# Performance work log

Measured on AMD Instinct MI355X. Metric: run time of the kernel, lower is better.

The kernel has to match this reference:

```python
import jax, jax.numpy as jnp
import numpy as np

B, S, D = 8, 2048, 256
MASK_FILL = -1e9


def setup_inputs() -> dict:
    key = jax.random.key(0)
    kq, kk, kv = jax.random.split(key, 3)
    query = jax.random.normal(kq, (B, S, D), dtype=jnp.float32)
    k_ = jax.random.normal(kk, (B, S, D), dtype=jnp.float32)
    value = jax.random.normal(kv, (B, S, D), dtype=jnp.float32)
    # causal mask: True = masked (gets -1e9), broadcast over batch
    causal = jnp.triu(jnp.ones((S, S), dtype=bool), k=1)
    mask = jnp.broadcast_to(causal, (B, S, S))
    return {"query": query, "key": k_, "value": value, "mask": mask}


def reference(query, key, value, mask):
    d = jnp.asarray(query.shape[-1], dtype=query.dtype)
    # (B,S,S) = bmm(Q, K^T) / sqrt(D)
    attention = jnp.einsum('bqd,bkd->bqk', query, key) / jnp.sqrt(d)
    attention = jnp.where(mask, jnp.asarray(MASK_FILL, attention.dtype), attention)
    attention = jax.nn.softmax(attention, axis=2)
    # dropout p=0.0 -> identity
    out = jnp.einsum('bqk,bkd->bqd', attention, value)
    return out, attention
```

## Files before the change

kernel.cpp:

```cpp
#include <hip/hip_runtime.h>
#include <hip/hip_bf16.h>

typedef __attribute__((ext_vector_type(4))) float  f32x4;
typedef __attribute__((ext_vector_type(8))) __bf16 bf16x8;

constexpr int Bn = 8, Sn = 2048, Dn = 256;
#define SCALE 0.0625f

__device__ float  g_lpart[(size_t)Bn * Sn * 16];
__device__ __bf16 g_vt[(size_t)Bn * Dn * Sn];
__device__ __bf16 g_praw[(size_t)Bn * Sn * Sn];

__device__ __forceinline__ f32x4 mfma_bf16(bf16x8 a, bf16x8 b, f32x4 c) {
  return __builtin_amdgcn_mfma_f32_16x16x32_bf16(a, b, c, 0, 0, 0);
}

__device__ __forceinline__ bf16x8 cvt8(const float* p) {
  const f32x4* q = (const f32x4*)p;
  f32x4 u0 = q[0], u1 = q[1];
  bf16x8 r;
#pragma unroll
  for (int j = 0; j < 4; ++j) { r[j] = (__bf16)u0[j]; r[4 + j] = (__bf16)u1[j]; }
  return r;
}

__global__ __launch_bounds__(512) void k_qkvt(const float* __restrict__ Q,
                                              const float* __restrict__ K,
                                              const float* __restrict__ V) {
  __shared__ __align__(16) char lds[34816];
  int tid = threadIdx.x;
  int bx = blockIdx.x;

  if (bx < 1024) {
    __bf16 (*t)[65] = reinterpret_cast<__bf16(*)[65]>(lds);
    int b = bx >> 7, rem = bx & 127;
    int s0 = (rem >> 2) << 6, d0 = (rem & 3) << 6;
#pragma unroll
    for (int i = 0; i < 8; ++i) {
      int idx = tid + (i << 9);
      int r = idx >> 6, c = idx & 63;
      t[r][c] = (__bf16)V[((size_t)(b * Sn + s0 + r) << 8) + d0 + c];
    }
    __syncthreads();
#pragma unroll
    for (int i = 0; i < 8; ++i) {
      int idx = tid + (i << 9);
      int r = idx >> 6, c = idx & 63;
      g_vt[((size_t)(b * Dn + d0 + r) << 11) + s0 + c] = t[c][r];
    }
    return;
  }

  __bf16 (*Ab)[64] = reinterpret_cast<__bf16(*)[64]>(lds);
  __bf16 (*Bb)[64] = reinterpret_cast<__bf16(*)[64]>(lds + 16384);
  __bf16 (*pbuf)[136] = reinterpret_cast<__bf16(*)[136]>(lds);

  int w = tid >> 6, lane = tid & 63, g = lane >> 4, c = lane & 15;
  int mi = w >> 2, ni = w & 3;
  int bq = bx - 1024;
  int b = bq & 7;
  int idx = bq >> 3;
  int mt = 15 - (idx >> 4), nt = idx & 15;
  if (nt > mt) return;

  int grow0 = mt << 7, gcol0 = nt << 7;
  const float* Qb = Q + (size_t)(b * Sn) * Dn;
  const float* Kb = K + (size_t)(b * Sn) * Dn;

  int sr = tid >> 2, u0 = (tid & 3) << 1;
  const float* qs = Qb + (size_t)(grow0 + sr) * Dn + (u0 << 3);
  const float* ks = Kb + (size_t)(gcol0 + sr) * Dn + (u0 << 3);
  int su0 = (u0 ^ (sr & 7)) << 3, su1 = ((u0 + 1) ^ (sr & 7)) << 3;

  f32x4 acc[4][2];
#pragma unroll
  for (int m2 = 0; m2 < 4; ++m2)
#pragma unroll
    for (int n2 = 0; n2 < 2; ++n2) acc[m2][n2] = {0.f, 0.f, 0.f, 0.f};

  bf16x8 qa0 = cvt8(qs), qa1 = cvt8(qs + 8);
  bf16x8 ka0 = cvt8(ks), ka1 = cvt8(ks + 8);

  for (int kb = 0; kb < 4; ++kb) {
    *reinterpret_cast<bf16x8*>(&Ab[sr][su0]) = qa0;
    *reinterpret_cast<bf16x8*>(&Ab[sr][su1]) = qa1;
    *reinterpret_cast<bf16x8*>(&Bb[sr][su0]) = ka0;
    *reinterpret_cast<bf16x8*>(&Bb[sr][su1]) = ka1;
    __syncthreads();

    if (kb + 1 < 4) {
      int k0 = (kb + 1) << 6;
      qa0 = cvt8(qs + k0);
      qa1 = cvt8(qs + k0 + 8);
      ka0 = cvt8(ks + k0);
      ka1 = cvt8(ks + k0 + 8);
    }

#pragma unroll
    for (int dk = 0; dk < 2; ++dk) {
      bf16x8 af[4], bfr[2];
#pragma unroll
      for (int m2 = 0; m2 < 4; ++m2) {
        int rr = (mi << 6) + (m2 << 4) + c;
        int uu = (g + (dk << 2)) ^ (rr & 7);
        af[m2] = *reinterpret_cast<const bf16x8*>(&Ab[rr][uu << 3]);
      }
#pragma unroll
      for (int n2 = 0; n2 < 2; ++n2) {
        int rr = (ni << 5) + (n2 << 4) + c;
        int uu = (g + (dk << 2)) ^ (rr & 7);
        bfr[n2] = *reinterpret_cast<const bf16x8*>(&Bb[rr][uu << 3]);
      }
#pragma unroll
      for (int m2 = 0; m2 < 4; ++m2)
#pragma unroll
        for (int n2 = 0; n2 < 2; ++n2)
          acc[m2][n2] = mfma_bf16(af[m2], bfr[n2], acc[m2][n2]);
    }
    __syncthreads();
  }

  bool diag = (nt == mt);
#pragma unroll
  for (int m2 = 0; m2 < 4; ++m2) {
#pragma unroll
    for (int r = 0; r < 4; ++r) {
      int row_l = (mi << 6) + (m2 << 4) + (g << 2) + r;
#pragma unroll
      for (int n2 = 0; n2 < 2; ++n2) {
        int col_l = (ni << 5) + (n2 << 4) + c;
        float e = (!diag || col_l <= row_l) ? __expf(acc[m2][n2][r] * SCALE) : 0.f;
        pbuf[row_l][col_l] = (__bf16)e;
      }
    }
  }
  __syncthreads();

  {
    int r = tid >> 2, q = tid & 3;
    __bf16* dst =
        g_praw + ((size_t)b << 22) + ((size_t)(grow0 + r) << 11) + gcol0 + (q << 5);
    float s = 0.f;
#pragma unroll
    for (int i = 0; i < 4; ++i) {
      bf16x8 vv = *reinterpret_cast<const bf16x8*>(&pbuf[r][(q << 5) + (i << 3)]);
      *reinterpret_cast<bf16x8*>(dst + (i << 3)) = vv;
#pragma unroll
      for (int e = 0; e < 8; ++e) s += (float)vv[e];
    }
    s += __shfl_xor(s, 1, 64);
    s += __shfl_xor(s, 2, 64);
    if (q == 0) g_lpart[((size_t)b * Sn + grow0 + r) * 16 + nt] = s;
  }
}

__global__ __launch_bounds__(512, 4) void k_pv(float* __restrict__ P,
                                               float* __restrict__ O) {
  __shared__ __align__(16) __bf16 abuf[2][64][64];
  __shared__ __align__(16) __bf16 vbuf[2][128][64];
  __shared__ float linv_s[64];
  int tid = threadIdx.x;
  int w = tid >> 6, lane = tid & 63, g = lane >> 4, c = lane & 15;
  int mi = w >> 2, ni = w & 3;
  int b = blockIdx.x & 7;
  int idx = blockIdx.x >> 3;
  int dh = idx & 1;
  int mt = 31 - (idx >> 1);
  int row0 = mt << 6;
  int nc = mt + 1;
  const __bf16* prb = g_praw + ((size_t)b << 22);
  const __bf16* vtb = g_vt + ((size_t)(b * Dn + (dh << 7)) << 11);
  float* Pb = P + ((size_t)b << 22);

  if (tid < 64) {
    const f32x4* p = reinterpret_cast<const f32x4*>(
        g_lpart + ((size_t)(b << 11) + row0 + tid) * 16);
    f32x4 s = (p[0] + p[1]) + (p[2] + p[3]);
    linv_s[tid] = 1.f / ((s[0] + s[1]) + (s[2] + s[3]));
  }

  int sr = tid >> 3, su = tid & 7;
  const __bf16* sp = prb + ((size_t)(row0 + sr) << 11) + (su << 3);
  float* spw = Pb + ((size_t)(row0 + sr) << 11) + (su << 3);
  int swu = (su ^ (sr & 7)) << 3;
  int vr = tid >> 2, vu = (tid & 3) << 1;
  const __bf16* vpp = vtb + ((size_t)vr << 11) + (vu << 3);
  int swv0 = (vu ^ (vr & 7)) << 3, swv1 = ((vu + 1) ^ (vr & 7)) << 3;

  f32x4 acc[2][2];
#pragma unroll
  for (int m2 = 0; m2 < 2; ++m2)
#pragma unroll
    for (int n2 = 0; n2 < 2; ++n2) acc[m2][n2] = {0.f, 0.f, 0.f, 0.f};

  bf16x8 pr = *reinterpret_cast<const bf16x8*>(sp);
  bf16x8 vt0 = *reinterpret_cast<const bf16x8*>(vpp);
  bf16x8 vt1 = *reinterpret_cast<const bf16x8*>(vpp + 8);

  __syncthreads();
  float slv = linv_s[sr];

  for (int j = 0; j < nc; ++j) {
    int jb = j & 1;
    *reinterpret_cast<bf16x8*>(&abuf[jb][sr][swu]) = pr;
    *reinterpret_cast<bf16x8*>(&vbuf[jb][vr][swv0]) = vt0;
    *reinterpret_cast<bf16x8*>(&vbuf[jb][vr][swv1]) = vt1;
    if ((j >> 4) == dh) {
      f32x4 p0, p1;
#pragma unroll
      for (int e = 0; e < 4; ++e) {
        p0[e] = (float)pr[e] * slv;
        p1[e] = (float)pr[4 + e] * slv;
      }
      float* pw = spw + ((size_t)j << 6);
      *reinterpret_cast<f32x4*>(pw) = p0;
      *reinterpret_cast<f32x4*>(pw + 4) = p1;
    }
    __syncthreads();

    if (j + 1 < nc) {
      const __bf16* sp2 = sp + ((size_t)(j + 1) << 6);
      const __bf16* vp2 = vpp + ((size_t)(j + 1) << 6);
      pr = *reinterpret_cast<const bf16x8*>(sp2);
      vt0 = *reinterpret_cast<const bf16x8*>(vp2);
      vt1 = *reinterpret_cast<const bf16x8*>(vp2 + 8);
    }

#pragma unroll
    for (int kk = 0; kk < 2; ++kk) {
      int ua = (kk << 2) + g;
      int ar0 = (mi << 5) + c, ar1 = ar0 + 16;
      bf16x8 a0 = *reinterpret_cast<const bf16x8*>(
          &abuf[jb][ar0][(ua ^ (ar0 & 7)) << 3]);
      bf16x8 a1 = *reinterpret_cast<const bf16x8*>(
          &abuf[jb][ar1][(ua ^ (ar1 & 7)) << 3]);
      int dr0 = (ni << 5) + c, dr1 = dr0 + 16;
      bf16x8 b0 = *reinterpret_cast<const bf16x8*>(
          &vbuf[jb][dr0][(ua ^ (dr0 & 7)) << 3]);
      bf16x8 b1 = *reinterpret_cast<const bf16x8*>(
          &vbuf[jb][dr1][(ua ^ (dr1 & 7)) << 3]);
      acc[0][0] = mfma_bf16(a0, b0, acc[0][0]);
      acc[0][1] = mfma_bf16(a0, b1, acc[0][1]);
      acc[1][0] = mfma_bf16(a1, b0, acc[1][0]);
      acc[1][1] = mfma_bf16(a1, b1, acc[1][1]);
    }
  }

  {
    int zs = nc << 6, hlo = dh << 10;
    if (zs < hlo) zs = hlo;
    int zend = hlo + 1024;
    float* prow = Pb + ((size_t)(row0 + sr) << 11);
    f32x4 z = {0.f, 0.f, 0.f, 0.f};
    for (int col = zs + (su << 2); col < zend; col += 32)
      *reinterpret_cast<f32x4*>(prow + col) = z;
  }

#pragma unroll
  for (int m2 = 0; m2 < 2; ++m2)
#pragma unroll
    for (int n2 = 0; n2 < 2; ++n2)
#pragma unroll
      for (int r = 0; r < 4; ++r) {
        int rl = (mi << 5) + (m2 << 4) + (g << 2) + r;
        O[((size_t)(b * Sn + row0 + rl) << 8) + (dh << 7) + (ni << 5) +
          (n2 << 4) + c] = acc[m2][n2][r] * linv_s[rl];
      }
}

extern "C" void kernel_launch(void* const* d_in, const int* in_sizes, int n_in,
                              void* d_out, int out_size, void* d_ws, size_t ws_size,
                              hipStream_t stream) {
  const float* Q = (const float*)d_in[0];
  const float* K = (const float*)d_in[1];
  const float* V = (const float*)d_in[2];

  float* out  = (float*)d_out;
  float* attn = out + (size_t)Bn * Sn * Dn;

  hipLaunchKernelGGL(k_qkvt, dim3(3072), dim3(512), 0, stream, Q, K, V);
  hipLaunchKernelGGL(k_pv, dim3(512), dim3(512), 0, stream, attn, out);
}
```

Before: 86.64 us.

## Widen QK^T tiles to 128x256 with 1024-thread blocks and split loaders

The QK^T/exp kernel now computes 128x256 score tiles with 16 waves per block instead of 128x128 tiles with 8 waves. Half of the threads stage Q and the other half stage the wider K tile, so each Q tile is loaded and converted once per 256 columns instead of once per 128. The causal mask is now applied per element using global coordinates for any tile that crosses the diagonal, and the row-sum reduction is widened to 8 lanes. This reduces redundant Q traffic and block count, at the cost of more wasted work on tiles that straddle the diagonal, larger LDS use, and lower occupancy from 1024-thread blocks. It also changes how partial row sums are indexed, which the unseen PV kernel must match.

```diff
diff --git a/kernel.cpp b/kernel.cpp
--- a/kernel.cpp
+++ b/kernel.cpp
@@ -24,10 +24,10 @@
   return r;
 }
 
-__global__ __launch_bounds__(512) void k_qkvt(const float* __restrict__ Q,
-                                              const float* __restrict__ K,
-                                              const float* __restrict__ V) {
-  __shared__ __align__(16) char lds[34816];
+__global__ __launch_bounds__(1024) void k_qkvt(const float* __restrict__ Q,
+                                               const float* __restrict__ K,
+                                               const float* __restrict__ V) {
+  __shared__ __align__(16) char lds[67584];
   int tid = threadIdx.x;
   int bx = blockIdx.x;
 
@@ -36,91 +36,128 @@
     int b = bx >> 7, rem = bx & 127;
     int s0 = (rem >> 2) << 6, d0 = (rem & 3) << 6;
 #pragma unroll
-    for (int i = 0; i < 8; ++i) {
-      int idx = tid + (i << 9);
+    for (int i = 0; i < 4; ++i) {
+      int idx = tid + (i << 10);
       int r = idx >> 6, c = idx & 63;
       t[r][c] = (__bf16)V[((size_t)(b * Sn + s0 + r) << 8) + d0 + c];
     }
     __syncthreads();
 #pragma unroll
-    for (int i = 0; i < 8; ++i) {
-      int idx = tid + (i << 9);
+    for (int i = 0; i < 4; ++i) {
+      int idx = tid + (i << 10);
       int r = idx >> 6, c = idx & 63;
       g_vt[((size_t)(b * Dn + d0 + r) << 11) + s0 + c] = t[c][r];
     }
     return;
   }
 
-  __bf16 (*Ab)[64] = reinterpret_cast<__bf16(*)[64]>(lds);
-  __bf16 (*Bb)[64] = reinterpret_cast<__bf16(*)[64]>(lds + 16384);
-  __bf16 (*pbuf)[136] = reinterpret_cast<__bf16(*)[136]>(lds);
-
   int w = tid >> 6, lane = tid & 63, g = lane >> 4, c = lane & 15;
-  int mi = w >> 2, ni = w & 3;
+  int mi = w >> 3, ni = w & 7;
   int bq = bx - 1024;
   int b = bq & 7;
   int idx = bq >> 3;
-  int mt = 15 - (idx >> 4), nt = idx & 15;
-  if (nt > mt) return;
-
-  int grow0 = mt << 7, gcol0 = nt << 7;
+  int nt = idx & 7, mt = 15 - (idx >> 3);
+  if (2 * nt > mt) return;
+
+  __bf16 (*Ab)[64] = reinterpret_cast<__bf16(*)[64]>(lds);
+  __bf16 (*Bb)[64] = reinterpret_cast<__bf16(*)[64]>(lds + 16384);
+  __bf16 (*pbuf)[264] = reinterpret_cast<__bf16(*)[264]>(lds);
+
+  int grow0 = mt << 7, gcol0 = nt << 8;
+  bool needmask = (gcol0 + 255) > grow0;
   const float* Qb = Q + (size_t)(b * Sn) * Dn;
   const float* Kb = K + (size_t)(b * Sn) * Dn;
 
-  int sr = tid >> 2, u0 = (tid & 3) << 1;
-  const float* qs = Qb + (size_t)(grow0 + sr) * Dn + (u0 << 3);
-  const float* ks = Kb + (size_t)(gcol0 + sr) * Dn + (u0 << 3);
-  int su0 = (u0 ^ (sr & 7)) << 3, su1 = ((u0 + 1) ^ (sr & 7)) << 3;
-
   f32x4 acc[4][2];
 #pragma unroll
   for (int m2 = 0; m2 < 4; ++m2)
 #pragma unroll
     for (int n2 = 0; n2 < 2; ++n2) acc[m2][n2] = {0.f, 0.f, 0.f, 0.f};
 
-  bf16x8 qa0 = cvt8(qs), qa1 = cvt8(qs + 8);
-  bf16x8 ka0 = cvt8(ks), ka1 = cvt8(ks + 8);
-
-  for (int kb = 0; kb < 4; ++kb) {
-    *reinterpret_cast<bf16x8*>(&Ab[sr][su0]) = qa0;
-    *reinterpret_cast<bf16x8*>(&Ab[sr][su1]) = qa1;
-    *reinterpret_cast<bf16x8*>(&Bb[sr][su0]) = ka0;
-    *reinterpret_cast<bf16x8*>(&Bb[sr][su1]) = ka1;
-    __syncthreads();
-
-    if (kb + 1 < 4) {
-      int k0 = (kb + 1) << 6;
-      qa0 = cvt8(qs + k0);
-      qa1 = cvt8(qs + k0 + 8);
-      ka0 = cvt8(ks + k0);
-      ka1 = cvt8(ks + k0 + 8);
-    }
-
-#pragma unroll
-    for (int dk = 0; dk < 2; ++dk) {
-      bf16x8 af[4], bfr[2];
-#pragma unroll
-      for (int m2 = 0; m2 < 4; ++m2) {
-        int rr = (mi << 6) + (m2 << 4) + c;
-        int uu = (g + (dk << 2)) ^ (rr & 7);
-        af[m2] = *reinterpret_cast<const bf16x8*>(&Ab[rr][uu << 3]);
-      }
-#pragma unroll
-      for (int n2 = 0; n2 < 2; ++n2) {
-        int rr = (ni << 5) + (n2 << 4) + c;
-        int uu = (g + (dk << 2)) ^ (rr & 7);
-        bfr[n2] = *reinterpret_cast<const bf16x8*>(&Bb[rr][uu << 3]);
-      }
-#pragma unroll
-      for (int m2 = 0; m2 < 4; ++m2)
-#pragma unroll
-        for (int n2 = 0; n2 < 2; ++n2)
-          acc[m2][n2] = mfma_bf16(af[m2], bfr[n2], acc[m2][n2]);
-    }
-    __syncthreads();
-  }
-
-  bool diag = (nt == mt);
+  if (tid < 512) {
+    int sr = tid >> 2, u0 = (tid & 3) << 1;
+    const float* qs = Qb + (size_t)(grow0 + sr) * Dn + (u0 << 3);
+    int su0 = (u0 ^ (sr & 7)) << 3, su1 = ((u0 + 1) ^ (sr & 7)) << 3;
+    bf16x8 qa0 = cvt8(qs), qa1 = cvt8(qs + 8);
+    for (int kb = 0; kb < 4; ++kb) {
+      *reinterpret_cast<bf16x8*>(&Ab[sr][su0]) = qa0;
+      *reinterpret_cast<bf16x8*>(&Ab[sr][su1]) = qa1;
+      __syncthreads();
+      if (kb + 1 < 4) {
+        int k0 = (kb + 1) << 6;
+        qa0 = cvt8(qs + k0);
+        qa1 = cvt8(qs + k0 + 8);
+      }
+#pragma unroll
+      for (int dk = 0; dk < 2; ++dk) {
+        bf16x8 af[4], bfr[2];
+#pragma unroll
+        for (int m2 = 0; m2 < 4; ++m2) {
+          int rr = (mi << 6) + (m2 << 4) + c;
+          int uu = (g + (dk << 2)) ^ (rr & 7);
+          af[m2] = *reinterpret_cast<const bf16x8*>(&Ab[rr][uu << 3]);
+        }
+#pragma unroll
+        for (int n2 = 0; n2 < 2; ++n2) {
+          int rr = (ni << 5) + (n2 << 4) + c;
+          int uu = (g + (dk << 2)) ^ (rr & 7);
+          bfr[n2] = *reinterpret_cast<const bf16x8*>(&Bb[rr][uu << 3]);
+        }
+#pragma unroll
+        for (int m2 = 0; m2 < 4; ++m2)
+#pragma unroll
+          for (int n2 = 0; n2 < 2; ++n2)
+            acc[m2][n2] = mfma_bf16(af[m2], bfr[n2], acc[m2][n2]);
+      }
+      __syncthreads();
+    }
+  } else {
+    int t2 = tid - 512;
+    int sr = t2 >> 1, u0 = (t2 & 1) << 2;
+    const float* ks = Kb + (size_t)(gcol0 + sr) * Dn + (u0 << 3);
+    int sw[4];
+#pragma unroll
+    for (int e = 0; e < 4; ++e) sw[e] = ((u0 + e) ^ (sr & 7)) << 3;
+    bf16x8 ka0 = cvt8(ks), ka1 = cvt8(ks + 8), ka2 = cvt8(ks + 16),
+           ka3 = cvt8(ks + 24);
+    for (int kb = 0; kb < 4; ++kb) {
+      *reinterpret_cast<bf16x8*>(&Bb[sr][sw[0]]) = ka0;
+      *reinterpret_cast<bf16x8*>(&Bb[sr][sw[1]]) = ka1;
+      *reinterpret_cast<bf16x8*>(&Bb[sr][sw[2]]) = ka2;
+      *reinterpret_cast<bf16x8*>(&Bb[sr][sw[3]]) = ka3;
+      __syncthreads();
+      if (kb + 1 < 4) {
+        int k0 = (kb + 1) << 6;
+        ka0 = cvt8(ks + k0);
+        ka1 = cvt8(ks + k0 + 8);
+        ka2 = cvt8(ks + k0 + 16);
+        ka3 = cvt8(ks + k0 + 24);
+      }
+#pragma unroll
+      for (int dk = 0; dk < 2; ++dk) {
+        bf16x8 af[4], bfr[2];
+#pragma unroll
+        for (int m2 = 0; m2 < 4; ++m2) {
+          int rr = (mi << 6) + (m2 << 4) + c;
+          int uu = (g + (dk << 2)) ^ (rr & 7);
+          af[m2] = *reinterpret_cast<const bf16x8*>(&Ab[rr][uu << 3]);
+        }
+#pragma unroll
+        for (int n2 = 0; n2 < 2; ++n2) {
+          int rr = (ni << 5) + (n2 << 4) + c;
+          int uu = (g + (dk << 2)) ^ (rr & 7);
+          bfr[n2] = *reinterpret_cast<const bf16x8*>(&Bb[rr][uu << 3]);
+        }
+#pragma unroll
+        for (int m2 = 0; m2 < 4; ++m2)
+#pragma unroll
+          for (int n2 = 0; n2 < 2; ++n2)
+            acc[m2][n2] = mfma_bf16(af[m2], bfr[n2], acc[m2][n2]);
+      }
+      __syncthreads();
+    }
+  }
+
 #pragma unroll
   for (int m2 = 0; m2 < 4; ++m2) {
 #pragma unroll
@@ -129,7 +166,9 @@
 #pragma unroll
       for (int n2 = 0; n2 < 2; ++n2) {
         int col_l = (ni << 5) + (n2 << 4) + c;
-        float e = (!diag || col_l <= row_l) ? __expf(acc[m2][n2][r] * SCALE) : 0.f;
+        float e = (!needmask || (gcol0 + col_l) <= (grow0 + row_l))
+                      ? __expf(acc[m2][n2][r] * SCALE)
+                      : 0.f;
         pbuf[row_l][col_l] = (__bf16)e;
       }
     }
@@ -137,7 +176,7 @@
   __syncthreads();
 
   {
-    int r = tid >> 2, q = tid & 3;
+    int r = tid >> 3, q = tid & 7;
     __bf16* dst =
         g_praw + ((size_t)b << 22) + ((size_t)(grow0 + r) << 11) + gcol0 + (q << 5);
     float s = 0.f;
@@ -150,6 +189,7 @@
     }
     s += __shfl_xor(s, 1, 64);
     s += __shfl_xor(s, 2, 64);
+    s += __shfl_xor(s, 4, 64);
     if (q == 0) g_lpart[((size_t)b * Sn + grow0 + r) * 16 + nt] = s;
   }
 }
@@ -278,6 +318,6 @@
   float* out  = (float*)d_out;
   float* attn = out + (size_t)Bn * Sn * Dn;
 
-  hipLaunchKernelGGL(k_qkvt, dim3(3072), dim3(512), 0, stream, Q, K, V);
+  hipLaunchKernelGGL(k_qkvt, dim3(2048), dim3(1024), 0, stream, Q, K, V);
   hipLaunchKernelGGL(k_pv, dim3(512), dim3(512), 0, stream, attn, out);
 }
```

After: 106.4 us. 1.23x slower.
